# Kernel tuning notes

Hardware: AMD Instinct MI355X
Metric: run time of the kernel (lower is better)

The kernel has to match this reference:

```python
import jax, jax.numpy as jnp
import numpy as np

N_NODES = 100000
N_EDGES = 6400000
DIM = 8


def setup_inputs() -> dict:
    key = jax.random.key(0)
    k1, k2, k3, k4 = jax.random.split(key, 4)
    state_input = jax.random.normal(k1, (N_NODES, DIM), dtype=jnp.float32)
    row = jax.random.randint(k2, (N_EDGES,), 0, N_NODES, dtype=jnp.int64)
    col = jax.random.randint(k3, (N_EDGES,), 0, N_NODES, dtype=jnp.int64)
    edge_weights = jax.random.uniform(k4, (N_EDGES,), dtype=jnp.float32)
    return {"state_input": state_input, "row": row, "col": col,
            "edge_weights": edge_weights}


def reference(state_input, row, col, edge_weights):
    # f equation (self term), per-dim: f_i(x) = -x_i
    self_diff = -state_input  # [N, dim]

    # gather endpoint features: interact_input = cat([x[col], x[row]], -1) -> [E, 2*dim]
    x_col = state_input[col]  # [E, dim]
    x_row = state_input[row]  # [E, dim]

    # g equation (pairwise term), per-dim: g_i = x_2_i - x_1_i  (row minus col)
    interact_diff = x_row - x_col  # [E, dim]

    # weight by edge weight and scatter-sum onto target nodes (col)
    messages = interact_diff * edge_weights[:, None]  # [E, dim]
    agg = jax.ops.segment_sum(messages, col, num_segments=state_input.shape[0])

    total_diff_signal = self_diff + agg  # [N, dim]
    return total_diff_signal
```

## Files before the change

### kernel.cpp

```cpp
#include <hip/hip_runtime.h>

#define N_NODES 100000
#define DIM 8
#define NB 128
#define BSHIFT 7
#define NBUCKETS ((N_NODES + NB - 1) / NB)
#define LSROW (NBUCKETS + 1)
#define G1 2048
#define ESPAN_MAX 3328
#define CAP 9728
#define NPER 10

__global__ void init_neg_kernel(const float* __restrict__ x,
                                float* __restrict__ out, int n4) {
    int i = blockIdx.x * blockDim.x + threadIdx.x;
    if (i < n4) {
        float4 v = reinterpret_cast<const float4*>(x)[i];
        float4 o; o.x = -v.x; o.y = -v.y; o.z = -v.z; o.w = -v.w;
        reinterpret_cast<float4*>(out)[i] = o;
    }
}

__global__ void edge_scatter_atomic(const float* __restrict__ x,
                                    const int* __restrict__ row,
                                    const int* __restrict__ col,
                                    const float* __restrict__ w,
                                    float* __restrict__ out, int nE) {
    int e = blockIdx.x * blockDim.x + threadIdx.x;
    if (e >= nE) return;
    int r = row[e], c = col[e];
    float we = w[e];
    const float4* xr = reinterpret_cast<const float4*>(x + (size_t)r * DIM);
    const float4* xc = reinterpret_cast<const float4*>(x + (size_t)c * DIM);
    float4 a0 = xr[0], a1 = xr[1], b0 = xc[0], b1 = xc[1];
    float* o = out + (size_t)c * DIM;
    atomicAdd(o + 0, (a0.x - b0.x) * we); atomicAdd(o + 1, (a0.y - b0.y) * we);
    atomicAdd(o + 2, (a0.z - b0.z) * we); atomicAdd(o + 3, (a0.w - b0.w) * we);
    atomicAdd(o + 4, (a1.x - b1.x) * we); atomicAdd(o + 5, (a1.y - b1.y) * we);
    atomicAdd(o + 6, (a1.z - b1.z) * we); atomicAdd(o + 7, (a1.w - b1.w) * we);
}


__global__ __launch_bounds__(256) void hist_scan_kernel(const int* __restrict__ col,
                                                        int nE, int espan,
                                                        unsigned* __restrict__ L) {
    __shared__ unsigned cnt[NBUCKETS];
    __shared__ unsigned part[256];
    int t = threadIdx.x, blk = blockIdx.x;
    long e0 = (long)blk * espan;
    long rem = (long)nE - e0;
    int n = (int)(rem > (long)espan ? espan : (rem < 0 ? 0 : rem));

    for (int i = t; i < NBUCKETS; i += 256) cnt[i] = 0;
    __syncthreads();
    for (int k = t; k < n; k += 256)
        atomicAdd(&cnt[((unsigned)col[e0 + k]) >> BSHIFT], 1u);
    __syncthreads();

    unsigned v[4], s = 0;
    #pragma unroll
    for (int j = 0; j < 4; ++j) {
        int b = 4 * t + j;
        v[j] = (b < NBUCKETS) ? cnt[b] : 0u;
        s += v[j];
    }
    part[t] = s; __syncthreads();
    for (int off = 1; off < 256; off <<= 1) {
        unsigned u = (t >= off) ? part[t - off] : 0u;
        __syncthreads();
        part[t] += u; __syncthreads();
    }
    unsigned base = part[t] - s;
    size_t lrow = (size_t)blk * LSROW;
    #pragma unroll
    for (int j = 0; j < 4; ++j) {
        int b = 4 * t + j;
        if (b < NBUCKETS) { L[lrow + b] = base; base += v[j]; }
    }
    if (t == 255) L[lrow + NBUCKETS] = part[255];
}

__global__ void transpose_kernel(const unsigned* __restrict__ in,
                                 unsigned* __restrict__ outp, int R, int C) {
    __shared__ unsigned tile[32][33];
    int tx = threadIdx.x, ty = threadIdx.y;
    int c0 = blockIdx.x * 32, r0 = blockIdx.y * 32;
    #pragma unroll
    for (int j = 0; j < 32; j += 8) {
        int r = r0 + ty + j, c = c0 + tx;
        if (r < R && c < C) tile[ty + j][tx] = in[(size_t)r * C + c];
    }
    __syncthreads();
    #pragma unroll
    for (int j = 0; j < 32; j += 8) {
        int c = c0 + ty + j, r = r0 + tx;
        if (r < R && c < C) outp[(size_t)c * R + r] = tile[tx][ty + j];
    }
}

__global__ __launch_bounds__(1024) void col_scan_kernel(const unsigned* __restrict__ LT,
                                                        unsigned* __restrict__ OT,
                                                        unsigned* __restrict__ bucketTotal) {
    __shared__ unsigned part[1024];
    int b = blockIdx.x, t = threadIdx.x;
    const unsigned* r0 = LT + (size_t)b * G1;
    const unsigned* r1 = LT + (size_t)(b + 1) * G1;
    unsigned c0 = r1[2 * t] - r0[2 * t];
    unsigned c1 = r1[2 * t + 1] - r0[2 * t + 1];
    part[t] = c0 + c1; __syncthreads();
    for (int off = 1; off < 1024; off <<= 1) {
        unsigned u = (t >= off) ? part[t - off] : 0u;
        __syncthreads();
        part[t] += u; __syncthreads();
    }
    unsigned ex = part[t] - (c0 + c1);
    OT[(size_t)b * G1 + 2 * t]     = ex;
    OT[(size_t)b * G1 + 2 * t + 1] = ex + c0;
    if (t == 1023) bucketTotal[b] = part[1023];
}

__global__ __launch_bounds__(1024) void bucket_scan_kernel(const unsigned* __restrict__ bucketTotal,
                                                           unsigned* __restrict__ bucketStart) {
    __shared__ unsigned sc[1024];
    int t = threadIdx.x;
    unsigned v = (t < NBUCKETS) ? bucketTotal[t] : 0u;
    sc[t] = v; __syncthreads();
    for (int off = 1; off < 1024; off <<= 1) {
        unsigned u = (t >= off) ? sc[t - off] : 0u;
        __syncthreads();
        sc[t] += u; __syncthreads();
    }
    if (t < NBUCKETS) bucketStart[t] = sc[t] - v;
    if (t == NBUCKETS - 1) bucketStart[NBUCKETS] = sc[t];
}

__global__ void add_transpose_kernel(const unsigned* __restrict__ OT,
                                     const unsigned* __restrict__ bucketStart,
                                     unsigned* __restrict__ blockOffs) {
    __shared__ unsigned tile[32][33];
    int tx = threadIdx.x, ty = threadIdx.y;
    int blk0 = blockIdx.x * 32, b0 = blockIdx.y * 32;
    #pragma unroll
    for (int j = 0; j < 32; j += 8) {
        int b = b0 + ty + j, blk = blk0 + tx;
        if (b < NBUCKETS && blk < G1)
            tile[ty + j][tx] = OT[(size_t)b * G1 + blk] + bucketStart[b];
    }
    __syncthreads();
    #pragma unroll
    for (int j = 0; j < 32; j += 8) {
        int blk = blk0 + ty + j, b = b0 + tx;
        if (b < NBUCKETS && blk < G1)
            blockOffs[(size_t)blk * NBUCKETS + b] = tile[tx][ty + j];
    }
}

__global__ __launch_bounds__(512) void scatter2_kernel(
        const int* __restrict__ row,
        const int* __restrict__ col,
        const float* __restrict__ w,
        int nE, int espan,
        const unsigned* __restrict__ L,
        const unsigned* __restrict__ blockOffs,
        uint2* __restrict__ payloadA) {
    __shared__ uint2 stage[ESPAN_MAX];
    __shared__ unsigned short sbkt[ESPAN_MAX];
    __shared__ unsigned cur[NBUCKETS];
    __shared__ unsigned diff[NBUCKETS];
    int t = threadIdx.x;
    int p = blockIdx.x;
    int v = (p & 7) * (G1 / 8) + (p >> 3);
    long e0 = (long)v * espan;
    long rem = (long)nE - e0;
    int n = (int)(rem > (long)espan ? espan : (rem < 0 ? 0 : rem));
    size_t lrow = (size_t)v * LSROW;

    for (int i = t; i < NBUCKETS; i += 512) {
        unsigned lv = L[lrow + i];
        cur[i]  = lv;
        diff[i] = blockOffs[(size_t)v * NBUCKETS + i] - lv;
    }
    __syncthreads();

    for (int k = t; k < n; k += 512) {
        unsigned c = (unsigned)col[e0 + k];
        unsigned b = c >> BSHIFT;
        unsigned pos = atomicAdd(&cur[b], 1u);
        stage[pos] = make_uint2(((unsigned)row[e0 + k] << BSHIFT) | (c & (NB - 1)),
                                __float_as_uint(w[e0 + k]));
        sbkt[pos] = (unsigned short)b;
    }
    __syncthreads();

    for (int k = t; k < n; k += 512) {
        unsigned b = sbkt[k];
        payloadA[diff[b] + (unsigned)k] = stage[k];
    }
}

__global__ __launch_bounds__(1024) void bucket_sort_gather_kernel(
        const float* __restrict__ x,
        const uint2* __restrict__ payloadA,
        const unsigned* __restrict__ bucketStart,
        float* __restrict__ out) {
    __shared__ uint2 stage[CAP];
    __shared__ unsigned cnt[NB];
    __shared__ unsigned scanb[NB];
    __shared__ unsigned exs[NB + 1];
    int b = blockIdx.x, t = threadIdx.x;
    int e0 = (int)bucketStart[b], e1 = (int)bucketStart[b + 1];
    int n = e1 - e0;

    if (t < NB) cnt[t] = 0;
    __syncthreads();

    if (n <= CAP) {
        uint2 regs[NPER];
        #pragma unroll
        for (int j = 0; j < NPER; ++j) {
            int k = (j << 10) + t;
            if (k < n) {
                uint2 p = payloadA[e0 + k];
                regs[j] = p;
                atomicAdd(&cnt[p.x & (NB - 1)], 1u);
            }
        }
        __syncthreads();
        if (t < NB) scanb[t] = cnt[t];
        __syncthreads();
        for (int off = 1; off < NB; off <<= 1) {
            unsigned v = 0;
            if (t < NB && t >= off) v = scanb[t - off];
            __syncthreads();
            if (t < NB) scanb[t] += v;
            __syncthreads();
        }
        if (t < NB) {
            unsigned ex = scanb[t] - cnt[t];
            exs[t] = ex;
            cnt[t] = ex;
        }
        if (t == 0) exs[NB] = (unsigned)n;
        __syncthreads();

        #pragma unroll
        for (int j = 0; j < NPER; ++j) {
            int k = (j << 10) + t;
            if (k < n) {
                uint2 p = regs[j];
                unsigned node = p.x & (NB - 1);
                unsigned pos = atomicAdd(&cnt[node], 1u);
                stage[pos] = make_uint2(p.x >> BSHIFT, p.y);
            }
        }
        __syncthreads();

        int slot = t;
        int node = slot >> 3, d = slot & 7;
        int gn = b * NB + node;
        if (gn < N_NODES) {
            float xc = x[(size_t)gn * DIM + d];
            int e = (int)exs[node], eEnd = (int)exs[node + 1];
            float a0 = 0.f, a1 = 0.f;
            for (; e + 4 <= eEnd; e += 4) {
                uint2 p0 = stage[e];
                uint2 p1 = stage[e + 1];
                uint2 p2 = stage[e + 2];
                uint2 p3 = stage[e + 3];
                float s0 = x[(size_t)p0.x * DIM + d];
                float s1 = x[(size_t)p1.x * DIM + d];
                float s2 = x[(size_t)p2.x * DIM + d];
                float s3 = x[(size_t)p3.x * DIM + d];
                a0 += (s0 - xc) * __uint_as_float(p0.y);
                a1 += (s1 - xc) * __uint_as_float(p1.y);
                a0 += (s2 - xc) * __uint_as_float(p2.y);
                a1 += (s3 - xc) * __uint_as_float(p3.y);
            }
            for (; e < eEnd; ++e) {
                uint2 p = stage[e];
                a0 += (x[(size_t)p.x * DIM + d] - xc) * __uint_as_float(p.y);
            }
            out[(size_t)gn * DIM + d] = a0 + a1 - xc;
        }
    } else {
        for (int slot = t; slot < NB * DIM; slot += 1024) {
            int gn = b * NB + (slot >> 3);
            if (gn < N_NODES) {
                size_t gi = (size_t)b * NB * DIM + slot;
                out[gi] = -x[gi];
            }
        }
        __syncthreads();
        int d = t & 7, sub = t >> 3;
        for (int k = sub; k < n; k += 128) {
            uint2 p = payloadA[e0 + k];
            int node = (int)(p.x & (NB - 1));
            int r = (int)(p.x >> BSHIFT);
            int gn = b * NB + node;
            if (gn < N_NODES) {
                float xc = x[(size_t)gn * DIM + d];
                atomicAdd(&out[(size_t)gn * DIM + d],
                          (x[(size_t)r * DIM + d] - xc) * __uint_as_float(p.y));
            }
        }
    }
}

extern "C" void kernel_launch(void* const* d_in, const int* in_sizes, int n_in,
                              void* d_out, int out_size, void* d_ws, size_t ws_size,
                              hipStream_t stream) {
    const float* x   = (const float*)d_in[0];
    const int*   row = (const int*)d_in[1];
    const int*   col = (const int*)d_in[2];
    const float* w   = (const float*)d_in[3];
    float* out = (float*)d_out;
    int nE = in_sizes[1];
    int n4 = out_size / 4;

    int espan = (nE + G1 - 1) / G1;

    auto align256 = [](size_t v) { return (v + 255) & ~(size_t)255; };
    size_t off_payloadA  = 0;
    size_t off_L         = align256(off_payloadA + (size_t)nE * sizeof(uint2));
    size_t off_LT        = align256(off_L  + (size_t)G1 * LSROW * 4);
    size_t off_OT        = align256(off_LT + (size_t)LSROW * G1 * 4);
    size_t off_blockOffs = align256(off_OT + (size_t)NBUCKETS * G1 * 4);
    size_t off_total     = align256(off_blockOffs + (size_t)G1 * NBUCKETS * 4);
    size_t off_start     = align256(off_total + (size_t)NBUCKETS * 4);
    size_t need          = off_start + (size_t)(NBUCKETS + 1) * 4;

    if (ws_size < need || espan > ESPAN_MAX) {
        init_neg_kernel<<<(n4 + 255) / 256, 256, 0, stream>>>(x, out, n4);
        edge_scatter_atomic<<<(nE + 255) / 256, 256, 0, stream>>>(x, row, col, w, out, nE);
        return;
    }

    char* p = (char*)d_ws;
    uint2*    payloadA    = (uint2*)(p + off_payloadA);
    unsigned* L           = (unsigned*)(p + off_L);
    unsigned* LT          = (unsigned*)(p + off_LT);
    unsigned* OT          = (unsigned*)(p + off_OT);
    unsigned* blockOffs   = (unsigned*)(p + off_blockOffs);
    unsigned* bucketTotal = (unsigned*)(p + off_total);
    unsigned* bucketStart = (unsigned*)(p + off_start);

    hist_scan_kernel<<<G1, 256, 0, stream>>>(col, nE, espan, L);
    transpose_kernel<<<dim3((LSROW + 31) / 32, G1 / 32), dim3(32, 8), 0, stream>>>(
        L, LT, G1, LSROW);
    col_scan_kernel<<<NBUCKETS, 1024, 0, stream>>>(LT, OT, bucketTotal);
    bucket_scan_kernel<<<1, 1024, 0, stream>>>(bucketTotal, bucketStart);
    add_transpose_kernel<<<dim3(G1 / 32, (NBUCKETS + 31) / 32), dim3(32, 8), 0, stream>>>(
        OT, bucketStart, blockOffs);
    scatter2_kernel<<<G1, 512, 0, stream>>>(row, col, w, nE, espan, L,
                                            blockOffs, payloadA);
    bucket_sort_gather_kernel<<<NBUCKETS, 1024, 0, stream>>>(x, payloadA,
                                                             bucketStart, out);
}
```

Before: 106.7 us.

## Split bucket gather into half-bucket blocks with partial-sum reduce, vectorize edge loads

Each 128-node bucket is now handled by two 512-thread blocks, each covering half of the bucket's edges and writing partial sums to workspace. A new reduce kernel adds the two partials and subtracts x. The local sort keeps each element's rank from the counting atomic, so the second atomic pass is gone. The histogram and scatter passes read col/row/w with int4/int2 vector loads, espan is rounded up to a multiple of 4 so those loads stay aligned, and the histogram block order is interleaved. The aim is more blocks, less shared memory per block and higher occupancy, at the price of an extra kernel launch and partial-sum traffic.

```diff
diff --git a/kernel.cpp b/kernel.cpp
--- a/kernel.cpp
+++ b/kernel.cpp
@@ -8,8 +8,8 @@
 #define LSROW (NBUCKETS + 1)
 #define G1 2048
 #define ESPAN_MAX 3328
-#define CAP 9728
-#define NPER 10
+#define CAP_H 4800
+#define NPER_H 10
 
 __global__ void init_neg_kernel(const float* __restrict__ x,
                                 float* __restrict__ out, int n4) {
@@ -46,14 +46,26 @@
                                                         unsigned* __restrict__ L) {
     __shared__ unsigned cnt[NBUCKETS];
     __shared__ unsigned part[256];
-    int t = threadIdx.x, blk = blockIdx.x;
+    int t = threadIdx.x;
+    int p = blockIdx.x;
+    int blk = (p & 7) * (G1 / 8) + (p >> 3);
     long e0 = (long)blk * espan;
     long rem = (long)nE - e0;
     int n = (int)(rem > (long)espan ? espan : (rem < 0 ? 0 : rem));
 
     for (int i = t; i < NBUCKETS; i += 256) cnt[i] = 0;
     __syncthreads();
-    for (int k = t; k < n; k += 256)
+
+    const int4* col4 = reinterpret_cast<const int4*>(col + e0);
+    int nv = n >> 2;
+    for (int k = t; k < nv; k += 256) {
+        int4 c4 = col4[k];
+        atomicAdd(&cnt[((unsigned)c4.x) >> BSHIFT], 1u);
+        atomicAdd(&cnt[((unsigned)c4.y) >> BSHIFT], 1u);
+        atomicAdd(&cnt[((unsigned)c4.z) >> BSHIFT], 1u);
+        atomicAdd(&cnt[((unsigned)c4.w) >> BSHIFT], 1u);
+    }
+    for (int k = (nv << 2) + t; k < n; k += 256)
         atomicAdd(&cnt[((unsigned)col[e0 + k]) >> BSHIFT], 1u);
     __syncthreads();
 
@@ -182,7 +194,26 @@
     }
     __syncthreads();
 
-    for (int k = t; k < n; k += 512) {
+    const int2*   col2 = reinterpret_cast<const int2*>(col + e0);
+    const int2*   row2 = reinterpret_cast<const int2*>(row + e0);
+    const float2* w2   = reinterpret_cast<const float2*>(w + e0);
+    int nv = n >> 1;
+    for (int k = t; k < nv; k += 512) {
+        int2 c2 = col2[k];
+        int2 r2 = row2[k];
+        float2 wv = w2[k];
+        unsigned b0 = ((unsigned)c2.x) >> BSHIFT;
+        unsigned pos0 = atomicAdd(&cur[b0], 1u);
+        stage[pos0] = make_uint2(((unsigned)r2.x << BSHIFT) | ((unsigned)c2.x & (NB - 1)),
+                                 __float_as_uint(wv.x));
+        sbkt[pos0] = (unsigned short)b0;
+        unsigned b1 = ((unsigned)c2.y) >> BSHIFT;
+        unsigned pos1 = atomicAdd(&cur[b1], 1u);
+        stage[pos1] = make_uint2(((unsigned)r2.y << BSHIFT) | ((unsigned)c2.y & (NB - 1)),
+                                 __float_as_uint(wv.y));
+        sbkt[pos1] = (unsigned short)b1;
+    }
+    for (int k = (nv << 1) + t; k < n; k += 512) {
         unsigned c = (unsigned)col[e0 + k];
         unsigned b = c >> BSHIFT;
         unsigned pos = atomicAdd(&cur[b], 1u);
@@ -198,31 +229,40 @@
     }
 }
 
-__global__ __launch_bounds__(1024) void bucket_sort_gather_kernel(
+__global__ __launch_bounds__(512, 8) void bucket_half_kernel(
         const float* __restrict__ x,
         const uint2* __restrict__ payloadA,
         const unsigned* __restrict__ bucketStart,
-        float* __restrict__ out) {
-    __shared__ uint2 stage[CAP];
+        float* __restrict__ partials) {
+    __shared__ uint2 stage[CAP_H];
     __shared__ unsigned cnt[NB];
     __shared__ unsigned scanb[NB];
     __shared__ unsigned exs[NB + 1];
-    int b = blockIdx.x, t = threadIdx.x;
-    int e0 = (int)bucketStart[b], e1 = (int)bucketStart[b + 1];
-    int n = e1 - e0;
+    int i = blockIdx.x;
+    int b = i >> 1, h = i & 1;
+    int t = threadIdx.x;
+    int e0b = (int)bucketStart[b], e1b = (int)bucketStart[b + 1];
+    int n = e1b - e0b;
+    int n2 = n >> 1;
+    int hs = h ? n2 : 0;
+    int he = h ? n : n2;
+    int nh = he - hs;
+    int e0 = e0b + hs;
+    float* myp = partials + (size_t)i * (NB * DIM);
 
     if (t < NB) cnt[t] = 0;
     __syncthreads();
 
-    if (n <= CAP) {
-        uint2 regs[NPER];
+    if (nh <= CAP_H) {
+        uint2 regs[NPER_H];
+        unsigned short rk[NPER_H];
         #pragma unroll
-        for (int j = 0; j < NPER; ++j) {
-            int k = (j << 10) + t;
-            if (k < n) {
+        for (int j = 0; j < NPER_H; ++j) {
+            int k = (j << 9) + t;
+            if (k < nh) {
                 uint2 p = payloadA[e0 + k];
                 regs[j] = p;
-                atomicAdd(&cnt[p.x & (NB - 1)], 1u);
+                rk[j] = (unsigned short)atomicAdd(&cnt[p.x & (NB - 1)], 1u);
             }
         }
         __syncthreads();
@@ -235,75 +275,81 @@
             if (t < NB) scanb[t] += v;
             __syncthreads();
         }
-        if (t < NB) {
-            unsigned ex = scanb[t] - cnt[t];
-            exs[t] = ex;
-            cnt[t] = ex;
-        }
-        if (t == 0) exs[NB] = (unsigned)n;
+        if (t < NB) exs[t] = scanb[t] - cnt[t];
+        if (t == 0) exs[NB] = (unsigned)nh;
         __syncthreads();
 
         #pragma unroll
-        for (int j = 0; j < NPER; ++j) {
-            int k = (j << 10) + t;
-            if (k < n) {
+        for (int j = 0; j < NPER_H; ++j) {
+            int k = (j << 9) + t;
+            if (k < nh) {
                 uint2 p = regs[j];
-                unsigned node = p.x & (NB - 1);
-                unsigned pos = atomicAdd(&cnt[node], 1u);
-                stage[pos] = make_uint2(p.x >> BSHIFT, p.y);
+                stage[exs[p.x & (NB - 1)] + (unsigned)rk[j]] =
+                    make_uint2(p.x >> BSHIFT, p.y);
             }
         }
         __syncthreads();
 
-        int slot = t;
-        int node = slot >> 3, d = slot & 7;
-        int gn = b * NB + node;
-        if (gn < N_NODES) {
-            float xc = x[(size_t)gn * DIM + d];
-            int e = (int)exs[node], eEnd = (int)exs[node + 1];
-            float a0 = 0.f, a1 = 0.f;
-            for (; e + 4 <= eEnd; e += 4) {
-                uint2 p0 = stage[e];
-                uint2 p1 = stage[e + 1];
-                uint2 p2 = stage[e + 2];
-                uint2 p3 = stage[e + 3];
-                float s0 = x[(size_t)p0.x * DIM + d];
-                float s1 = x[(size_t)p1.x * DIM + d];
-                float s2 = x[(size_t)p2.x * DIM + d];
-                float s3 = x[(size_t)p3.x * DIM + d];
-                a0 += (s0 - xc) * __uint_as_float(p0.y);
-                a1 += (s1 - xc) * __uint_as_float(p1.y);
-                a0 += (s2 - xc) * __uint_as_float(p2.y);
-                a1 += (s3 - xc) * __uint_as_float(p3.y);
-            }
-            for (; e < eEnd; ++e) {
-                uint2 p = stage[e];
-                a0 += (x[(size_t)p.x * DIM + d] - xc) * __uint_as_float(p.y);
-            }
-            out[(size_t)gn * DIM + d] = a0 + a1 - xc;
-        }
-    } else {
-        for (int slot = t; slot < NB * DIM; slot += 1024) {
-            int gn = b * NB + (slot >> 3);
-            if (gn < N_NODES) {
-                size_t gi = (size_t)b * NB * DIM + slot;
-                out[gi] = -x[gi];
-            }
-        }
-        __syncthreads();
-        int d = t & 7, sub = t >> 3;
-        for (int k = sub; k < n; k += 128) {
-            uint2 p = payloadA[e0 + k];
-            int node = (int)(p.x & (NB - 1));
-            int r = (int)(p.x >> BSHIFT);
+        #pragma unroll
+        for (int s = 0; s < 2; ++s) {
+            int slot = t + (s << 9);
+            int node = slot >> 3, d = slot & 7;
             int gn = b * NB + node;
             if (gn < N_NODES) {
                 float xc = x[(size_t)gn * DIM + d];
-                atomicAdd(&out[(size_t)gn * DIM + d],
-                          (x[(size_t)r * DIM + d] - xc) * __uint_as_float(p.y));
+                int e = (int)exs[node], eEnd = (int)exs[node + 1];
+                float a0 = 0.f, a1 = 0.f;
+                for (; e + 4 <= eEnd; e += 4) {
+                    uint2 p0 = stage[e];
+                    uint2 p1 = stage[e + 1];
+                    uint2 p2 = stage[e + 2];
+                    uint2 p3 = stage[e + 3];
+                    float s0 = x[(size_t)p0.x * DIM + d];
+                    float s1 = x[(size_t)p1.x * DIM + d];
+                    float s2 = x[(size_t)p2.x * DIM + d];
+                    float s3 = x[(size_t)p3.x * DIM + d];
+                    a0 += (s0 - xc) * __uint_as_float(p0.y);
+                    a1 += (s1 - xc) * __uint_as_float(p1.y);
+                    a0 += (s2 - xc) * __uint_as_float(p2.y);
+                    a1 += (s3 - xc) * __uint_as_float(p3.y);
+                }
+                for (; e < eEnd; ++e) {
+                    uint2 p = stage[e];
+                    a0 += (x[(size_t)p.x * DIM + d] - xc) * __uint_as_float(p.y);
+                }
+                myp[slot] = a0 + a1;
+            } else {
+                myp[slot] = 0.f;
             }
         }
-    }
+    } else {
+        for (int s = t; s < NB * DIM; s += 512) myp[s] = 0.f;
+        __syncthreads();
+        int d = t & 7, sub = t >> 3;
+        for (int k = sub; k < nh; k += 64) {
+            uint2 p = payloadA[e0 + k];
+            int node = (int)(p.x & (NB - 1));
+            int gn = b * NB + node;
+            if (gn < N_NODES) {
+                float xc = x[(size_t)gn * DIM + d];
+                atomicAdd(&myp[node * DIM + d],
+                          (x[(size_t)(p.x >> BSHIFT) * DIM + d] - xc) * __uint_as_float(p.y));
+            }
+        }
+    }
+}
+
+__global__ __launch_bounds__(1024) void reduce_out_kernel(
+        const float* __restrict__ x,
+        const float* __restrict__ partials,
+        float* __restrict__ out) {
+    int b = blockIdx.x, t = threadIdx.x;
+    int gn = b * NB + (t >> 3);
+    if (gn >= N_NODES) return;
+    size_t gi = (size_t)b * (NB * DIM) + t;
+    out[gi] = partials[(size_t)(2 * b) * (NB * DIM) + t]
+            + partials[(size_t)(2 * b + 1) * (NB * DIM) + t]
+            - x[gi];
 }
 
 extern "C" void kernel_launch(void* const* d_in, const int* in_sizes, int n_in,
@@ -318,6 +364,7 @@
     int n4 = out_size / 4;
 
     int espan = (nE + G1 - 1) / G1;
+    espan = (espan + 3) & ~3;
 
     auto align256 = [](size_t v) { return (v + 255) & ~(size_t)255; };
     size_t off_payloadA  = 0;
@@ -327,7 +374,8 @@
     size_t off_blockOffs = align256(off_OT + (size_t)NBUCKETS * G1 * 4);
     size_t off_total     = align256(off_blockOffs + (size_t)G1 * NBUCKETS * 4);
     size_t off_start     = align256(off_total + (size_t)NBUCKETS * 4);
-    size_t need          = off_start + (size_t)(NBUCKETS + 1) * 4;
+    size_t off_partials  = align256(off_start + (size_t)(NBUCKETS + 1) * 4);
+    size_t need          = off_partials + (size_t)2 * NBUCKETS * NB * DIM * 4;
 
     if (ws_size < need || espan > ESPAN_MAX) {
         init_neg_kernel<<<(n4 + 255) / 256, 256, 0, stream>>>(x, out, n4);
@@ -343,6 +391,7 @@
     unsigned* blockOffs   = (unsigned*)(p + off_blockOffs);
     unsigned* bucketTotal = (unsigned*)(p + off_total);
     unsigned* bucketStart = (unsigned*)(p + off_start);
+    float*    partials    = (float*)(p + off_partials);
 
     hist_scan_kernel<<<G1, 256, 0, stream>>>(col, nE, espan, L);
     transpose_kernel<<<dim3((LSROW + 31) / 32, G1 / 32), dim3(32, 8), 0, stream>>>(
@@ -353,6 +402,7 @@
         OT, bucketStart, blockOffs);
     scatter2_kernel<<<G1, 512, 0, stream>>>(row, col, w, nE, espan, L,
                                             blockOffs, payloadA);
-    bucket_sort_gather_kernel<<<NBUCKETS, 1024, 0, stream>>>(x, payloadA,
-                                                             bucketStart, out);
-}
+    bucket_half_kernel<<<2 * NBUCKETS, 512, 0, stream>>>(x, payloadA,
+                                                         bucketStart, partials);
+    reduce_out_kernel<<<NBUCKETS, 1024, 0, stream>>>(x, partials, out);
+}
```

After: 104.1 us. -2.4%, faster.
